# Kernel tuning notes

Measured on AMD Instinct MI355X. Metric: run time of the kernel, lower is better.

The kernel has to match this reference:

```python
import jax, jax.numpy as jnp
import numpy as np

B, C, D, H, W = 8, 1, 160, 160, 160
SPATIAL_AXES = (2, 3, 4)  # axial, coronal, sagittal map to dims D, H, W


def setup_inputs() -> dict:
    key = jax.random.key(0)
    k1, _ = jax.random.split(key)
    x = jax.random.normal(k1, (B, C, D, H, W), dtype=jnp.float32)
    log_sigma = jnp.zeros((3,), dtype=jnp.float32)  # log(initial_sigma=1.0)
    return {"x": x, "log_sigma": log_sigma}


def reference(x, log_sigma):
    # For each spatial axis: adjacent-slice diff, squared distance summed over
    # channel + remaining spatial dims (per batch, per slice-pair), RBF kernel,
    # then -mean over (batch, slice-pairs). Equivalent to the original
    # sum_i(-mean_b(k_i)) / (n_slices - 1) since mean is linear.
    sigma = jnp.exp(log_sigma)
    total = jnp.float32(0.0)
    for i, ax in enumerate(SPATIAL_AXES):
        d = jnp.diff(x, axis=ax)  # [B, C, ...] with S-1 along ax
        reduce_dims = tuple(a for a in range(5) if a not in (0, ax))
        sq = jnp.sum(d * d, axis=reduce_dims)  # [B, S-1]
        k = jnp.exp(-sq / (2.0 * sigma[i] ** 2))
        total = total + (-jnp.mean(k))
    return total / jnp.float32(len(SPATIAL_AXES))
```

## Files before the change

### kernel.cpp

```cpp
#include <hip/hip_runtime.h>


constexpr int Wd4 = 40;
constexpr int SLICE4 = 6400;
constexpr long BSTR4 = 160L * 6400;
constexpr int NB = 8;
constexpr int NPAIR = 159;
constexpr int NKEY = 3 * NB * NPAIR;
constexpr int SLOT = 200;
constexpr int NBLK = NB * 160;
constexpr int PART_OFF = NBLK * SLOT;
constexpr int NFIN = 60;

__device__ __forceinline__ float sq4(const float4& a, const float4& c) {
    float e0 = a.x - c.x, e1 = a.y - c.y, e2 = a.z - c.z, e3 = a.w - c.w;
    return e0 * e0 + e1 * e1 + e2 * e2 + e3 * e3;
}

__global__ __launch_bounds__(320) void diff3_kernel(const float* __restrict__ x,
                                                    float* __restrict__ ws) {
    __shared__ float lds[1504];

    const int t = threadIdx.x;
    const int bid = blockIdx.x;
    const int b = bid / 160;
    const int r2 = bid % 160;
    const int ds = r2 / 5;
    const int hc = r2 % 5;
    const int d0 = ds * 5, h0 = hc * 32;
    const bool lastSeg = (ds == 31);

    const int c4 = t % 40;
    const int rp = t / 40;
    const int lane = t & 63;
    const int wv = t >> 6;
    const bool hOK = !(hc == 4 && rp == 7);
    const bool sOK = (c4 < 39);
    const bool fixB = (lane == 63) && sOK;

    const float4* base = (const float4*)x + (size_t)b * BSTR4 + (size_t)d0 * SLICE4
                       + (size_t)(h0 + 4 * rp) * Wd4 + c4;

    float aW[4] = {0.f, 0.f, 0.f, 0.f};
    float aH[4] = {0.f, 0.f, 0.f, 0.f};
    float aD[5] = {0.f, 0.f, 0.f, 0.f, 0.f};
    float4 p0, p1, p2, p3;

#pragma unroll
    for (int it = 0; it < 5; ++it) {
        const float4* sp = base + it * SLICE4;
        const float4 v0 = sp[0];
        const float4 v1 = sp[Wd4];
        const float4 v2 = sp[2 * Wd4];
        const float4 v3 = sp[3 * Wd4];
        float4 hv;
        if (hOK) hv = sp[4 * Wd4];
        float bx0 = 0.f, bx1 = 0.f, bx2 = 0.f, bx3 = 0.f;
        if (fixB) {
            bx0 = ((const float*)(sp))[4];
            bx1 = ((const float*)(sp + Wd4))[4];
            bx2 = ((const float*)(sp + 2 * Wd4))[4];
            bx3 = ((const float*)(sp + 3 * Wd4))[4];
        }
        float s0 = __shfl_down(v0.x, 1, 64); if (fixB) s0 = bx0;
        float s1 = __shfl_down(v1.x, 1, 64); if (fixB) s1 = bx1;
        float s2 = __shfl_down(v2.x, 1, 64); if (fixB) s2 = bx2;
        float s3 = __shfl_down(v3.x, 1, 64); if (fixB) s3 = bx3;

        float dw;
        dw = v0.y - v0.x; aW[0] += dw * dw;
        dw = v0.z - v0.y; aW[1] += dw * dw;
        dw = v0.w - v0.z; aW[2] += dw * dw;
        dw = v1.y - v1.x; aW[0] += dw * dw;
        dw = v1.z - v1.y; aW[1] += dw * dw;
        dw = v1.w - v1.z; aW[2] += dw * dw;
        dw = v2.y - v2.x; aW[0] += dw * dw;
        dw = v2.z - v2.y; aW[1] += dw * dw;
        dw = v2.w - v2.z; aW[2] += dw * dw;
        dw = v3.y - v3.x; aW[0] += dw * dw;
        dw = v3.z - v3.y; aW[1] += dw * dw;
        dw = v3.w - v3.z; aW[2] += dw * dw;
        if (sOK) {
            dw = s0 - v0.w; aW[3] += dw * dw;
            dw = s1 - v1.w; aW[3] += dw * dw;
            dw = s2 - v2.w; aW[3] += dw * dw;
            dw = s3 - v3.w; aW[3] += dw * dw;
        }
        aH[0] += sq4(v1, v0);
        aH[1] += sq4(v2, v1);
        aH[2] += sq4(v3, v2);
        if (hOK) aH[3] += sq4(hv, v3);
        if (it > 0)
            aD[it - 1] += sq4(v0, p0) + sq4(v1, p1) + sq4(v2, p2) + sq4(v3, p3);
        p0 = v0; p1 = v1; p2 = v2; p3 = v3;
    }
    if (!lastSeg) {
        const float4* sp = base + 5 * SLICE4;
        aD[4] = sq4(sp[0], p0) + sq4(sp[Wd4], p1) + sq4(sp[2 * Wd4], p2) + sq4(sp[3 * Wd4], p3);
    }

#pragma unroll
    for (int j = 0; j < 4; ++j) lds[(4 * rp + j) * 41 + c4] = aH[j];
#pragma unroll
    for (int j = 0; j < 5; ++j) {
        float dd = aD[j];
        for (int off = 32; off > 0; off >>= 1) dd += __shfl_down(dd, off, 64);
        if (lane == 0) lds[1472 + j * 5 + wv] = dd;
    }
    __syncthreads();
    float hsum = 0.f, dsum = 0.f;
    if (t < 32) {
        const float* src = &lds[t * 41];
        for (int i = 0; i < 40; ++i) hsum += src[i];
    }
    if (t < 5) {
        for (int w2 = 0; w2 < 5; ++w2) dsum += lds[1472 + t * 5 + w2];
    }
    __syncthreads();
#pragma unroll
    for (int j = 0; j < 4; ++j) lds[(4 * c4 + j) * 9 + rp] = aW[j];
    __syncthreads();
    float wsum = 0.f;
    if (t < 160) {
        const float* src = &lds[t * 9];
        for (int i = 0; i < 8; ++i) wsum += src[i];
    }
    float* slot = ws + (size_t)bid * SLOT;
    if (t < 5)   slot[t] = dsum;
    if (t < 32)  slot[5 + t] = hsum;
    if (t < 160) slot[37 + t] = wsum;
}

__global__ __launch_bounds__(64) void reduce_kernel(const float* __restrict__ ws,
                                                    const float* __restrict__ log_sigma,
                                                    float* __restrict__ part) {
    const int gk = blockIdx.x * 64 + threadIdx.x;
    float kv = 0.f;
    if (gk < NKEY) {
        const int a = gk / (NB * NPAIR);
        const int rem = gk % (NB * NPAIR);
        const int b = rem / NPAIR;
        const int k = rem % NPAIR;
        const float f = -0.5f * expf(-2.f * log_sigma[a]);
        const float* bb = ws + (size_t)b * 160 * SLOT;
        float val = 0.f;
        if (a == 0) {
            const int ds = k / 5, j = k % 5;
            const float* p = bb + (size_t)(ds * 5) * SLOT + j;
            for (int hc = 0; hc < 5; ++hc) val += p[hc * SLOT];
        } else if (a == 1) {
            const int hc = k / 32, kk = k % 32;
            const float* p = bb + (size_t)hc * SLOT + 5 + kk;
            for (int ds = 0; ds < 32; ++ds) val += p[(size_t)(ds * 5) * SLOT];
        } else {
            const float* p = bb + 37 + k;
            for (int i = 0; i < 160; ++i) val += p[(size_t)i * SLOT];
        }
        kv = expf(val * f);
    }
    for (int off = 32; off > 0; off >>= 1) kv += __shfl_down(kv, off, 64);
    if (threadIdx.x == 0) part[blockIdx.x] = kv;
}

__global__ __launch_bounds__(64) void final_kernel(const float* __restrict__ part,
                                                   float* __restrict__ out) {
    float v = (threadIdx.x < NFIN) ? part[threadIdx.x] : 0.f;
    for (int off = 32; off > 0; off >>= 1) v += __shfl_down(v, off, 64);
    if (threadIdx.x == 0) out[0] = -v / (float)NKEY;
}

extern "C" void kernel_launch(void* const* d_in, const int* in_sizes, int n_in,
                              void* d_out, int out_size, void* d_ws, size_t ws_size,
                              hipStream_t stream) {
    const float* x = (const float*)d_in[0];
    const float* log_sigma = (const float*)d_in[1];
    float* out = (float*)d_out;
    float* ws = (float*)d_ws;

    diff3_kernel<<<NBLK, 320, 0, stream>>>(x, ws);
    reduce_kernel<<<NFIN, 64, 0, stream>>>(ws, log_sigma, ws + PART_OFF);
    final_kernel<<<1, 64, 0, stream>>>(ws + PART_OFF, out);
}
```

Measured before the change: 197.1 us.

## Fuse slice-sum reduction and RBF finalize into main kernel via atomics

Each block now atomically accumulates its per-slice partial sums straight into a compact per-(axis,batch,pair) buffer. A completion counter lets the last block apply the RBF exponentials and the final mean, which removes the separate reduce and final kernels. A small zeroing kernel is launched first to clear the accumulators and the counter. This drops one launch and the strided gather over a large workspace, at the cost of global atomic contention and a serialized tail in the last block.

```diff
diff --git a/kernel.cpp b/kernel.cpp
--- a/kernel.cpp
+++ b/kernel.cpp
@@ -7,19 +7,23 @@
 constexpr int NB = 8;
 constexpr int NPAIR = 159;
 constexpr int NKEY = 3 * NB * NPAIR;
-constexpr int SLOT = 200;
 constexpr int NBLK = NB * 160;
-constexpr int PART_OFF = NBLK * SLOT;
-constexpr int NFIN = 60;
 
 __device__ __forceinline__ float sq4(const float4& a, const float4& c) {
     float e0 = a.x - c.x, e1 = a.y - c.y, e2 = a.z - c.z, e3 = a.w - c.w;
     return e0 * e0 + e1 * e1 + e2 * e2 + e3 * e3;
 }
 
+__global__ __launch_bounds__(1024) void zero_ws_kernel(float* __restrict__ ws) {
+    for (int i = threadIdx.x; i < NKEY + 1; i += 1024) ws[i] = 0.f;
+}
+
 __global__ __launch_bounds__(320) void diff3_kernel(const float* __restrict__ x,
-                                                    float* __restrict__ ws) {
+                                                    const float* __restrict__ log_sigma,
+                                                    float* __restrict__ ws,
+                                                    float* __restrict__ out) {
     __shared__ float lds[1504];
+    __shared__ int isLast;
 
     const int t = threadIdx.x;
     const int bid = blockIdx.x;
@@ -125,48 +129,38 @@
         const float* src = &lds[t * 9];
         for (int i = 0; i < 8; ++i) wsum += src[i];
     }
-    float* slot = ws + (size_t)bid * SLOT;
-    if (t < 5)   slot[t] = dsum;
-    if (t < 32)  slot[5 + t] = hsum;
-    if (t < 160) slot[37 + t] = wsum;
-}
 
-__global__ __launch_bounds__(64) void reduce_kernel(const float* __restrict__ ws,
-                                                    const float* __restrict__ log_sigma,
-                                                    float* __restrict__ part) {
-    const int gk = blockIdx.x * 64 + threadIdx.x;
-    float kv = 0.f;
-    if (gk < NKEY) {
-        const int a = gk / (NB * NPAIR);
-        const int rem = gk % (NB * NPAIR);
-        const int b = rem / NPAIR;
-        const int k = rem % NPAIR;
-        const float f = -0.5f * expf(-2.f * log_sigma[a]);
-        const float* bb = ws + (size_t)b * 160 * SLOT;
-        float val = 0.f;
-        if (a == 0) {
-            const int ds = k / 5, j = k % 5;
-            const float* p = bb + (size_t)(ds * 5) * SLOT + j;
-            for (int hc = 0; hc < 5; ++hc) val += p[hc * SLOT];
-        } else if (a == 1) {
-            const int hc = k / 32, kk = k % 32;
-            const float* p = bb + (size_t)hc * SLOT + 5 + kk;
-            for (int ds = 0; ds < 32; ++ds) val += p[(size_t)(ds * 5) * SLOT];
-        } else {
-            const float* p = bb + 37 + k;
-            for (int i = 0; i < 160; ++i) val += p[(size_t)i * SLOT];
+    if (t < 5 && (d0 + t) < NPAIR)   atomicAdd(&ws[b * NPAIR + d0 + t], dsum);
+    if (t < 32 && (h0 + t) < NPAIR)  atomicAdd(&ws[NB * NPAIR + b * NPAIR + h0 + t], hsum);
+    if (t < 160 && t < NPAIR)        atomicAdd(&ws[2 * NB * NPAIR + b * NPAIR + t], wsum);
+    __syncthreads();
+
+    if (t == 0) {
+        __threadfence();
+        int old = atomicAdd((int*)(ws + NKEY), 1);
+        isLast = (old == NBLK - 1) ? 1 : 0;
+    }
+    __syncthreads();
+
+    if (isLast) {
+        __threadfence();
+        const float f0 = -0.5f * __expf(-2.f * log_sigma[0]);
+        const float f1 = -0.5f * __expf(-2.f * log_sigma[1]);
+        const float f2 = -0.5f * __expf(-2.f * log_sigma[2]);
+        float acc = 0.f;
+        for (int i = t; i < NKEY; i += 320) {
+            float val = atomicAdd(&ws[i], 0.f);
+            float f = (i < NB * NPAIR) ? f0 : ((i < 2 * NB * NPAIR) ? f1 : f2);
+            acc += expf(val * f);
         }
-        kv = expf(val * f);
+        for (int off = 32; off > 0; off >>= 1) acc += __shfl_down(acc, off, 64);
+        if (lane == 0) lds[wv] = acc;
+        __syncthreads();
+        if (t == 0) {
+            float s = lds[0] + lds[1] + lds[2] + lds[3] + lds[4];
+            out[0] = -s / (float)NKEY;
+        }
     }
-    for (int off = 32; off > 0; off >>= 1) kv += __shfl_down(kv, off, 64);
-    if (threadIdx.x == 0) part[blockIdx.x] = kv;
-}
-
-__global__ __launch_bounds__(64) void final_kernel(const float* __restrict__ part,
-                                                   float* __restrict__ out) {
-    float v = (threadIdx.x < NFIN) ? part[threadIdx.x] : 0.f;
-    for (int off = 32; off > 0; off >>= 1) v += __shfl_down(v, off, 64);
-    if (threadIdx.x == 0) out[0] = -v / (float)NKEY;
 }
 
 extern "C" void kernel_launch(void* const* d_in, const int* in_sizes, int n_in,
@@ -177,7 +171,6 @@
     float* out = (float*)d_out;
     float* ws = (float*)d_ws;
 
-    diff3_kernel<<<NBLK, 320, 0, stream>>>(x, ws);
-    reduce_kernel<<<NFIN, 64, 0, stream>>>(ws, log_sigma, ws + PART_OFF);
-    final_kernel<<<1, 64, 0, stream>>>(ws + PART_OFF, out);
+    zero_ws_kernel<<<1, 1024, 0, stream>>>(ws);
+    diff3_kernel<<<NBLK, 320, 0, stream>>>(x, log_sigma, ws, out);
 }
```

Measured after the change: 227.9 us. 1.16x slower.

## Enlarge per-block H tile to 80 rows with 10 rows per thread

Applied to the files above, without the earlier changes.

Each block now covers 80 H rows instead of 32, and each thread processes 10 consecutive rows per slice instead of 4. This cuts the number of blocks from 1280 to 512 and reduces the redundant halo-row reload for the H diff. It also shrinks the workspace partial sums that reduce_kernel must gather, especially for the W axis (64 slots instead of 160). The cost is higher register pressure from the 10 float4 values plus 10 previous float4 kept per thread, and fewer blocks available for latency hiding.

```diff
diff --git a/kernel.cpp b/kernel.cpp
--- a/kernel.cpp
+++ b/kernel.cpp
@@ -7,8 +7,8 @@
 constexpr int NB = 8;
 constexpr int NPAIR = 159;
 constexpr int NKEY = 3 * NB * NPAIR;
-constexpr int SLOT = 200;
-constexpr int NBLK = NB * 160;
+constexpr int SLOT = 256;
+constexpr int NBLK = NB * 32 * 2;
 constexpr int PART_OFF = NBLK * SLOT;
 constexpr int NFIN = 60;
 
@@ -19,102 +19,95 @@
 
 __global__ __launch_bounds__(320) void diff3_kernel(const float* __restrict__ x,
                                                     float* __restrict__ ws) {
-    __shared__ float lds[1504];
+    __shared__ float lds[3320];
 
     const int t = threadIdx.x;
     const int bid = blockIdx.x;
-    const int b = bid / 160;
-    const int r2 = bid % 160;
-    const int ds = r2 / 5;
-    const int hc = r2 % 5;
-    const int d0 = ds * 5, h0 = hc * 32;
+    const int b = bid / 64;
+    const int r2 = bid % 64;
+    const int ds = r2 >> 1;
+    const int hg = r2 & 1;
+    const int d0 = ds * 5, h0 = hg * 80;
     const bool lastSeg = (ds == 31);
 
     const int c4 = t % 40;
     const int rp = t / 40;
     const int lane = t & 63;
     const int wv = t >> 6;
-    const bool hOK = !(hc == 4 && rp == 7);
     const bool sOK = (c4 < 39);
     const bool fixB = (lane == 63) && sOK;
+    const int hvOff = (hg == 1 && rp == 7) ? 9 * Wd4 : 10 * Wd4;
 
     const float4* base = (const float4*)x + (size_t)b * BSTR4 + (size_t)d0 * SLICE4
-                       + (size_t)(h0 + 4 * rp) * Wd4 + c4;
+                       + (size_t)(h0 + 10 * rp) * Wd4 + c4;
 
     float aW[4] = {0.f, 0.f, 0.f, 0.f};
-    float aH[4] = {0.f, 0.f, 0.f, 0.f};
-    float aD[5] = {0.f, 0.f, 0.f, 0.f, 0.f};
-    float4 p0, p1, p2, p3;
+    float aH[10], aD[5] = {0.f, 0.f, 0.f, 0.f, 0.f};
+#pragma unroll
+    for (int j = 0; j < 10; ++j) aH[j] = 0.f;
+    float4 p[10];
 
 #pragma unroll
     for (int it = 0; it < 5; ++it) {
         const float4* sp = base + it * SLICE4;
-        const float4 v0 = sp[0];
-        const float4 v1 = sp[Wd4];
-        const float4 v2 = sp[2 * Wd4];
-        const float4 v3 = sp[3 * Wd4];
-        float4 hv;
-        if (hOK) hv = sp[4 * Wd4];
-        float bx0 = 0.f, bx1 = 0.f, bx2 = 0.f, bx3 = 0.f;
+        float4 v[10];
+#pragma unroll
+        for (int j = 0; j < 10; ++j) v[j] = sp[j * Wd4];
+        const float4 hv = sp[hvOff];
+        float bx[10];
         if (fixB) {
-            bx0 = ((const float*)(sp))[4];
-            bx1 = ((const float*)(sp + Wd4))[4];
-            bx2 = ((const float*)(sp + 2 * Wd4))[4];
-            bx3 = ((const float*)(sp + 3 * Wd4))[4];
+            const float* fb = (const float*)sp;
+#pragma unroll
+            for (int j = 0; j < 10; ++j) bx[j] = fb[j * 160 + 4];
         }
-        float s0 = __shfl_down(v0.x, 1, 64); if (fixB) s0 = bx0;
-        float s1 = __shfl_down(v1.x, 1, 64); if (fixB) s1 = bx1;
-        float s2 = __shfl_down(v2.x, 1, 64); if (fixB) s2 = bx2;
-        float s3 = __shfl_down(v3.x, 1, 64); if (fixB) s3 = bx3;
 
-        float dw;
-        dw = v0.y - v0.x; aW[0] += dw * dw;
-        dw = v0.z - v0.y; aW[1] += dw * dw;
-        dw = v0.w - v0.z; aW[2] += dw * dw;
-        dw = v1.y - v1.x; aW[0] += dw * dw;
-        dw = v1.z - v1.y; aW[1] += dw * dw;
-        dw = v1.w - v1.z; aW[2] += dw * dw;
-        dw = v2.y - v2.x; aW[0] += dw * dw;
-        dw = v2.z - v2.y; aW[1] += dw * dw;
-        dw = v2.w - v2.z; aW[2] += dw * dw;
-        dw = v3.y - v3.x; aW[0] += dw * dw;
-        dw = v3.z - v3.y; aW[1] += dw * dw;
-        dw = v3.w - v3.z; aW[2] += dw * dw;
-        if (sOK) {
-            dw = s0 - v0.w; aW[3] += dw * dw;
-            dw = s1 - v1.w; aW[3] += dw * dw;
-            dw = s2 - v2.w; aW[3] += dw * dw;
-            dw = s3 - v3.w; aW[3] += dw * dw;
+#pragma unroll
+        for (int j = 0; j < 10; ++j) {
+            const float4 vj = v[j];
+            float s = __shfl_down(vj.x, 1, 64);
+            if (fixB) s = bx[j];
+            float dw;
+            dw = vj.y - vj.x; aW[0] += dw * dw;
+            dw = vj.z - vj.y; aW[1] += dw * dw;
+            dw = vj.w - vj.z; aW[2] += dw * dw;
+            if (sOK) { dw = s - vj.w; aW[3] += dw * dw; }
         }
-        aH[0] += sq4(v1, v0);
-        aH[1] += sq4(v2, v1);
-        aH[2] += sq4(v3, v2);
-        if (hOK) aH[3] += sq4(hv, v3);
-        if (it > 0)
-            aD[it - 1] += sq4(v0, p0) + sq4(v1, p1) + sq4(v2, p2) + sq4(v3, p3);
-        p0 = v0; p1 = v1; p2 = v2; p3 = v3;
+#pragma unroll
+        for (int j = 0; j < 9; ++j) aH[j] += sq4(v[j + 1], v[j]);
+        aH[9] += sq4(hv, v[9]);
+        if (it > 0) {
+            float dd = 0.f;
+#pragma unroll
+            for (int j = 0; j < 10; ++j) dd += sq4(v[j], p[j]);
+            aD[it - 1] += dd;
+        }
+#pragma unroll
+        for (int j = 0; j < 10; ++j) p[j] = v[j];
     }
     if (!lastSeg) {
         const float4* sp = base + 5 * SLICE4;
-        aD[4] = sq4(sp[0], p0) + sq4(sp[Wd4], p1) + sq4(sp[2 * Wd4], p2) + sq4(sp[3 * Wd4], p3);
+        float dd = 0.f;
+#pragma unroll
+        for (int j = 0; j < 10; ++j) dd += sq4(sp[j * Wd4], p[j]);
+        aD[4] = dd;
     }
 
 #pragma unroll
-    for (int j = 0; j < 4; ++j) lds[(4 * rp + j) * 41 + c4] = aH[j];
+    for (int j = 0; j < 10; ++j) lds[(10 * rp + j) * 41 + c4] = aH[j];
 #pragma unroll
     for (int j = 0; j < 5; ++j) {
         float dd = aD[j];
         for (int off = 32; off > 0; off >>= 1) dd += __shfl_down(dd, off, 64);
-        if (lane == 0) lds[1472 + j * 5 + wv] = dd;
+        if (lane == 0) lds[3280 + j * 8 + wv] = dd;
     }
     __syncthreads();
     float hsum = 0.f, dsum = 0.f;
-    if (t < 32) {
+    if (t < 80) {
         const float* src = &lds[t * 41];
         for (int i = 0; i < 40; ++i) hsum += src[i];
     }
     if (t < 5) {
-        for (int w2 = 0; w2 < 5; ++w2) dsum += lds[1472 + t * 5 + w2];
+        for (int w2 = 0; w2 < 5; ++w2) dsum += lds[3280 + t * 8 + w2];
     }
     __syncthreads();
 #pragma unroll
@@ -127,8 +120,8 @@
     }
     float* slot = ws + (size_t)bid * SLOT;
     if (t < 5)   slot[t] = dsum;
-    if (t < 32)  slot[5 + t] = hsum;
-    if (t < 160) slot[37 + t] = wsum;
+    if (t < 80)  slot[5 + t] = hsum;
+    if (t < 160) slot[85 + t] = wsum;
 }
 
 __global__ __launch_bounds__(64) void reduce_kernel(const float* __restrict__ ws,
@@ -142,19 +135,19 @@
         const int b = rem / NPAIR;
         const int k = rem % NPAIR;
         const float f = -0.5f * expf(-2.f * log_sigma[a]);
-        const float* bb = ws + (size_t)b * 160 * SLOT;
+        const float* bb = ws + (size_t)b * 64 * SLOT;
         float val = 0.f;
         if (a == 0) {
             const int ds = k / 5, j = k % 5;
-            const float* p = bb + (size_t)(ds * 5) * SLOT + j;
-            for (int hc = 0; hc < 5; ++hc) val += p[hc * SLOT];
+            const float* p = bb + (size_t)(ds * 2) * SLOT + j;
+            val = p[0] + p[SLOT];
         } else if (a == 1) {
-            const int hc = k / 32, kk = k % 32;
-            const float* p = bb + (size_t)hc * SLOT + 5 + kk;
-            for (int ds = 0; ds < 32; ++ds) val += p[(size_t)(ds * 5) * SLOT];
+            const int hg = k / 80, kh = k % 80;
+            const float* p = bb + (size_t)hg * SLOT + 5 + kh;
+            for (int ds = 0; ds < 32; ++ds) val += p[(size_t)(ds * 2) * SLOT];
         } else {
-            const float* p = bb + 37 + k;
-            for (int i = 0; i < 160; ++i) val += p[(size_t)i * SLOT];
+            const float* p = bb + 85 + k;
+            for (int i = 0; i < 64; ++i) val += p[(size_t)i * SLOT];
         }
         kv = expf(val * f);
     }
```

Result: slower. 258.3 us (+31.1%).
